# Optimization experiments

Measured on AMD Instinct MI355X. Metric: run time of the kernel, lower is better.

The kernel has to match this reference:

```python
import jax, jax.numpy as jnp
import numpy as np

B = 16384      # batch of samples
D = 65         # inps columns: 64 input spins + 1 output spin y
NA = 64        # auxiliary (threshold) spins
N = D + NA     # spins entering vspin expansion: 129
M = N + N * (N - 1) // 2  # degree-<=2 spin monomials: 8385
GAMMA = 1.0

# pairwise index pattern (i < j), computed once at trace time
_II, _JJ = np.triu_indices(N, k=1)


def batch_vspin(b):
    # b: [B, N] -> [B, N + N(N-1)/2]: linear terms then all pairwise products b_i*b_j (i<j)
    return jnp.concatenate([b, b[:, _II] * b[:, _JJ]], axis=-1)


def setup_inputs() -> dict:
    key = jax.random.key(0)
    k1, k2, k3, k4 = jax.random.split(key, 4)
    inps = jax.random.normal(k1, (B, D), dtype=jnp.float32)
    thresh_w = jax.random.normal(k2, (NA, D), dtype=jnp.float32) * 0.1
    thresh_b = jax.random.normal(k3, (NA,), dtype=jnp.float32) * 0.1
    main_w = jax.random.normal(k4, (1, M), dtype=jnp.float32) * 0.02
    return {"inps": inps, "thresh_w": thresh_w, "thresh_b": thresh_b, "main_w": main_w}


def reference(inps, thresh_w, thresh_b, main_w):
    inps = inps.astype(jnp.float32)
    x = inps[:, :-1]                      # [B, D-1]
    y = inps[:, -1:]                      # [B, 1]
    i_right = jnp.concatenate([x, y], axis=-1)    # [B, D]
    i_wrong = jnp.concatenate([x, -y], axis=-1)   # [B, D]

    w1 = i_right @ thresh_w.T + thresh_b          # [B, NA]
    w2 = i_wrong @ thresh_w.T + thresh_b          # [B, NA]
    t1 = jnp.tanh(GAMMA * w1)
    t2 = jnp.tanh(GAMMA * w2)

    b1 = jnp.concatenate([i_right, t1], axis=-1)  # [B, N]
    b2 = jnp.concatenate([i_wrong, t2], axis=-1)  # [B, N]
    v1 = batch_vspin(b1)                          # [B, M]
    v2 = batch_vspin(b2)                          # [B, M]

    diff = (v1 - v2) @ main_w.T + 1.0             # [B, 1]
    int_penalty = jnp.sum((GAMMA / 300.0) * ((1.0 - t1 ** 2) ** 2 + (1.0 - t2 ** 2) ** 2))
    neut_penalty = jnp.sum((t2 * w2 - t1 * w1) ** 2)
    return (diff, int_penalty, neut_penalty)
```

## Files before the change

### kernel.cpp

```cpp
#include <hip/hip_runtime.h>

#define B_SZ 16384
#define N_SP 129
#define GRID 1024
#define BLOCK 256

typedef _Float16 half8 __attribute__((ext_vector_type(8)));
typedef float float4v __attribute__((ext_vector_type(4)));

#define WS_TWY  6144
#define WS_QXY  6208
#define WS_QYT  6272
#define WS_LINT 6336
#define WS_LINY 6400
#define WS_P1   6464
#define WS_P2   7488

__device__ __forceinline__ int qidx(int i, int j) {
  return N_SP + i * (2 * N_SP - i - 1) / 2 + (j - i - 1);
}

__device__ __forceinline__ float fast_tanh(float x) {
  float xc = fminf(fmaxf(x, -15.f), 15.f);
  float e = __expf(2.f * xc);
  return 1.f - 2.f / (e + 1.f);
}

__global__ void setup_kernel(const float* __restrict__ mw, const float* __restrict__ tw,
                             float* __restrict__ wsf) {
  int t = blockIdx.x * blockDim.x + threadIdx.x;
  if (t < 12288) {
    int frag = t >> 9, e = t & 511;
    int lane = e >> 3, j = e & 7;
    int tbl = frag >> 3, tg = frag & 7;
    int kt = tg >> 2, g = tg & 3;
    int k = kt * 32 + (lane >> 4) * 8 + j;
    int n = (lane & 15) + 16 * g;
    float v;
    if (tbl == 0) {
      v = tw[n * 65 + k];
    } else if (tbl == 1) {
      v = mw[qidx(n, 65 + k)];
    } else {
      v = 0.f;
      if (n != k) {
        int a = n < k ? n : k, b = n < k ? k : n;
        v = mw[qidx(65 + a, 65 + b)];
      }
    }
    ((_Float16*)wsf)[t] = (_Float16)v;
  } else if (t < 12352) {
    int u = t - 12288; wsf[WS_TWY + u] = tw[u * 65 + 64];
  } else if (t < 12416) {
    int i = t - 12352; wsf[WS_QXY + i] = mw[qidx(i, 64)];
  } else if (t < 12480) {
    int u = t - 12416; wsf[WS_QYT + u] = mw[qidx(64, 65 + u)];
  } else if (t < 12544) {
    int u = t - 12480; wsf[WS_LINT + u] = mw[65 + u];
  } else if (t == 12544) {
    wsf[WS_LINY] = mw[64];
  }
}

__global__ __launch_bounds__(BLOCK, 4) void main_kernel(
    const float* __restrict__ inps, const float* __restrict__ tb,
    float* __restrict__ wsf, float* __restrict__ out) {
  __shared__ __align__(16) _Float16 s_frag[12288];
  __shared__ __align__(16) _Float16 s_x[1152];
  __shared__ __align__(16) _Float16 s_dt[1152];
  __shared__ float s_part[64];
  __shared__ float s_red[8];

  const int tid = threadIdx.x;
  const int l = tid & 63, wib = tid >> 6;
  const int b0 = blockIdx.x << 4;
  const int q = l >> 4, m = l & 15;
  const int u = (wib << 4) + m;

  {
    const float4* wsv = (const float4*)wsf;
    float4* dst = (float4*)s_frag;
#pragma unroll
    for (int i = 0; i < 6; i++) dst[tid + 256 * i] = wsv[tid + 256 * i];
  }
  const float twyv = wsf[WS_TWY + u];
  const float qxyv = wsf[WS_QXY + u];
  const float qytv = wsf[WS_QYT + u];
  const float lintv = wsf[WS_LINT + u];
  const float liny = wsf[WS_LINY];
  const float tbv = tb[u];

  {
    const float4* src4 = (const float4*)(inps + b0 * 65);
    float4 v = src4[tid];
#pragma unroll
    for (int c = 0; c < 4; c++) {
      unsigned idx = tid * 4 + c;
      unsigned row = idx / 65u, col = idx - row * 65u;
      s_x[row * 72 + col] = (_Float16)((const float*)&v)[c];
    }
    if (tid < 4) {
      float4 v2 = src4[256 + tid];
#pragma unroll
      for (int c = 0; c < 4; c++) {
        unsigned idx = (256 + tid) * 4 + c;
        unsigned row = idx / 65u, col = idx - row * 65u;
        s_x[row * 72 + col] = (_Float16)((const float*)&v2)[c];
      }
    }
  }
  __syncthreads();

  const half8* fragv = (const half8*)s_frag;

  half8 ax0 = *(const half8*)(s_x + m * 72 + q * 8);
  half8 ax1 = *(const half8*)(s_x + m * 72 + 32 + q * 8);

  float4v acc = {0.f, 0.f, 0.f, 0.f};
  acc = __builtin_amdgcn_mfma_f32_16x16x32_f16(ax0, fragv[(0 + wib) * 64 + l], acc, 0, 0, 0);
  acc = __builtin_amdgcn_mfma_f32_16x16x32_f16(ax1, fragv[(4 + wib) * 64 + l], acc, 0, 0, 0);

  float yv[4], dtv[4], stv[4];
  float pint = 0.f, pneut = 0.f;
#pragma unroll
  for (int r = 0; r < 4; r++) {
    yv[r] = (float)s_x[(q * 4 + r) * 72 + 64];
    float wpre = acc[r] + tbv;
    float w1 = wpre + twyv * yv[r];
    float w2 = wpre - twyv * yv[r];
    float t1 = fast_tanh(w1), t2 = fast_tanh(w2);
    dtv[r] = t1 - t2; stv[r] = t1 + t2;
    float a1 = 1.f - t1 * t1, a2 = 1.f - t2 * t2;
    pint += a1 * a1 + a2 * a2;
    float nv = t2 * w2 - t1 * w1;
    pneut += nv * nv;
    s_dt[(q * 4 + r) * 72 + u] = (_Float16)dtv[r];
  }
  __syncthreads();

  half8 ad0 = *(const half8*)(s_dt + m * 72 + q * 8);
  half8 ad1 = *(const half8*)(s_dt + m * 72 + 32 + q * 8);

  float4v rxt = {0.f, 0.f, 0.f, 0.f}, rtt = {0.f, 0.f, 0.f, 0.f};
  rxt = __builtin_amdgcn_mfma_f32_16x16x32_f16(ad0, fragv[(8 + wib) * 64 + l], rxt, 0, 0, 0);
  rxt = __builtin_amdgcn_mfma_f32_16x16x32_f16(ad1, fragv[(12 + wib) * 64 + l], rxt, 0, 0, 0);
  rtt = __builtin_amdgcn_mfma_f32_16x16x32_f16(ad0, fragv[(16 + wib) * 64 + l], rtt, 0, 0, 0);
  rtt = __builtin_amdgcn_mfma_f32_16x16x32_f16(ad1, fragv[(20 + wib) * 64 + l], rtt, 0, 0, 0);

  float creg[4];
#pragma unroll
  for (int r = 0; r < 4; r++) {
    float xv = (float)s_x[(q * 4 + r) * 72 + u];
    float c = xv * (2.f * yv[r] * qxyv + rxt[r])
            + yv[r] * stv[r] * qytv
            + 0.5f * stv[r] * rtt[r]
            + lintv * dtv[r];
    c += __shfl_xor(c, 1); c += __shfl_xor(c, 2);
    c += __shfl_xor(c, 4); c += __shfl_xor(c, 8);
    creg[r] = c;
  }
  if (m == 0) {
#pragma unroll
    for (int r = 0; r < 4; r++) s_part[wib * 16 + q * 4 + r] = creg[r];
  }

#pragma unroll
  for (int off = 1; off < 64; off <<= 1) {
    pint += __shfl_xor(pint, off);
    pneut += __shfl_xor(pneut, off);
  }
  if (l == 0) { s_red[wib] = pint; s_red[4 + wib] = pneut; }
  __syncthreads();

  if (tid < 16) {
    float c = s_part[tid] + s_part[16 + tid] + s_part[32 + tid] + s_part[48 + tid];
    float y = (float)s_x[tid * 72 + 64];
    out[b0 + tid] = 1.f + 2.f * y * liny + c;
  }
  if (tid == 0) {
    wsf[WS_P1 + blockIdx.x] = s_red[0] + s_red[1] + s_red[2] + s_red[3];
    wsf[WS_P2 + blockIdx.x] = s_red[4] + s_red[5] + s_red[6] + s_red[7];
  }
}

__global__ __launch_bounds__(1024) void reduce_kernel(const float* __restrict__ wsf,
                                                      float* __restrict__ out) {
  __shared__ float s[32];
  const int tid = threadIdx.x;
  float a = wsf[WS_P1 + tid];
  float b = wsf[WS_P2 + tid];
#pragma unroll
  for (int off = 1; off < 64; off <<= 1) {
    a += __shfl_xor(a, off);
    b += __shfl_xor(b, off);
  }
  const int w = tid >> 6, l = tid & 63;
  if (l == 0) { s[w] = a; s[16 + w] = b; }
  __syncthreads();
  if (tid == 0) {
    float sa = 0.f, sb = 0.f;
#pragma unroll
    for (int i = 0; i < 16; i++) { sa += s[i]; sb += s[16 + i]; }
    out[B_SZ] = sa * (1.f / 300.f);
    out[B_SZ + 1] = sb;
  }
}

extern "C" void kernel_launch(void* const* d_in, const int* in_sizes, int n_in,
                              void* d_out, int out_size, void* d_ws, size_t ws_size,
                              hipStream_t stream) {
  const float* inps = (const float*)d_in[0];
  const float* tw   = (const float*)d_in[1];
  const float* tb   = (const float*)d_in[2];
  const float* mw   = (const float*)d_in[3];
  float* out = (float*)d_out;
  float* wsf = (float*)d_ws;
  setup_kernel<<<50, 256, 0, stream>>>(mw, tw, wsf);
  main_kernel<<<GRID, BLOCK, 0, stream>>>(inps, tb, wsf, out);
  reduce_kernel<<<1, 1024, 0, stream>>>(wsf, out);
}
```

Baseline: 68.85 us.

## Fuse final reduction into main kernel via atomic ticket and async LDS loads

Removes the separate single-block reduce kernel. The last main-kernel block to finish, found through an atomic ticket counter, sums the per-block penalty partials itself. The fragment table now sits in device globals and is copied straight into LDS with global_load_lds, so it no longer passes through registers. This saves one kernel launch and its tail latency, at the cost of atomics and a global counter that must be reset correctly for every later call.

After: 87.24 us. +26.7%, slower.

```diff
diff --git a/kernel.cpp b/kernel.cpp
--- a/kernel.cpp
+++ b/kernel.cpp
@@ -8,13 +8,15 @@
 typedef _Float16 half8 __attribute__((ext_vector_type(8)));
 typedef float float4v __attribute__((ext_vector_type(4)));
 
-#define WS_TWY  6144
-#define WS_QXY  6208
-#define WS_QYT  6272
-#define WS_LINT 6336
-#define WS_LINY 6400
-#define WS_P1   6464
-#define WS_P2   7488
+__device__ __align__(16) _Float16 g_frag[12288];
+__device__ float g_twy[64];
+__device__ float g_qxy[64];
+__device__ float g_qyt[64];
+__device__ float g_lint[64];
+__device__ float g_liny_v;
+__device__ float g_p1[GRID];
+__device__ float g_p2[GRID];
+__device__ unsigned g_ticket = 0;
 
 __device__ __forceinline__ int qidx(int i, int j) {
   return N_SP + i * (2 * N_SP - i - 1) / 2 + (j - i - 1);
@@ -26,8 +28,7 @@
   return 1.f - 2.f / (e + 1.f);
 }
 
-__global__ void setup_kernel(const float* __restrict__ mw, const float* __restrict__ tw,
-                             float* __restrict__ wsf) {
+__global__ void setup_kernel(const float* __restrict__ mw, const float* __restrict__ tw) {
   int t = blockIdx.x * blockDim.x + threadIdx.x;
   if (t < 12288) {
     int frag = t >> 9, e = t & 511;
@@ -48,28 +49,29 @@
         v = mw[qidx(65 + a, 65 + b)];
       }
     }
-    ((_Float16*)wsf)[t] = (_Float16)v;
+    g_frag[t] = (_Float16)v;
   } else if (t < 12352) {
-    int u = t - 12288; wsf[WS_TWY + u] = tw[u * 65 + 64];
+    int u = t - 12288; g_twy[u] = tw[u * 65 + 64];
   } else if (t < 12416) {
-    int i = t - 12352; wsf[WS_QXY + i] = mw[qidx(i, 64)];
+    int i = t - 12352; g_qxy[i] = mw[qidx(i, 64)];
   } else if (t < 12480) {
-    int u = t - 12416; wsf[WS_QYT + u] = mw[qidx(64, 65 + u)];
+    int u = t - 12416; g_qyt[u] = mw[qidx(64, 65 + u)];
   } else if (t < 12544) {
-    int u = t - 12480; wsf[WS_LINT + u] = mw[65 + u];
+    int u = t - 12480; g_lint[u] = mw[65 + u];
   } else if (t == 12544) {
-    wsf[WS_LINY] = mw[64];
+    g_liny_v = mw[64];
   }
 }
 
 __global__ __launch_bounds__(BLOCK, 4) void main_kernel(
     const float* __restrict__ inps, const float* __restrict__ tb,
-    float* __restrict__ wsf, float* __restrict__ out) {
+    float* __restrict__ out) {
   __shared__ __align__(16) _Float16 s_frag[12288];
   __shared__ __align__(16) _Float16 s_x[1152];
   __shared__ __align__(16) _Float16 s_dt[1152];
   __shared__ float s_part[64];
   __shared__ float s_red[8];
+  __shared__ bool s_last;
 
   const int tid = threadIdx.x;
   const int l = tid & 63, wib = tid >> 6;
@@ -78,16 +80,20 @@
   const int u = (wib << 4) + m;
 
   {
-    const float4* wsv = (const float4*)wsf;
-    float4* dst = (float4*)s_frag;
-#pragma unroll
-    for (int i = 0; i < 6; i++) dst[tid + 256 * i] = wsv[tid + 256 * i];
-  }
-  const float twyv = wsf[WS_TWY + u];
-  const float qxyv = wsf[WS_QXY + u];
-  const float qytv = wsf[WS_QYT + u];
-  const float lintv = wsf[WS_LINT + u];
-  const float liny = wsf[WS_LINY];
+    const char* src = (const char*)g_frag;
+#pragma unroll
+    for (int i = 0; i < 6; i++) {
+      __builtin_amdgcn_global_load_lds(
+          (const __attribute__((address_space(1))) void*)(src + (tid + 256 * i) * 16),
+          (__attribute__((address_space(3))) void*)(s_frag + (wib * 64 + 256 * i) * 8),
+          16, 0, 0);
+    }
+  }
+  const float twyv = g_twy[u];
+  const float qxyv = g_qxy[u];
+  const float qytv = g_qyt[u];
+  const float lintv = g_lint[u];
+  const float liny = g_liny_v;
   const float tbv = tb[u];
 
   {
@@ -178,31 +184,35 @@
     out[b0 + tid] = 1.f + 2.f * y * liny + c;
   }
   if (tid == 0) {
-    wsf[WS_P1 + blockIdx.x] = s_red[0] + s_red[1] + s_red[2] + s_red[3];
-    wsf[WS_P2 + blockIdx.x] = s_red[4] + s_red[5] + s_red[6] + s_red[7];
-  }
-}
-
-__global__ __launch_bounds__(1024) void reduce_kernel(const float* __restrict__ wsf,
-                                                      float* __restrict__ out) {
-  __shared__ float s[32];
-  const int tid = threadIdx.x;
-  float a = wsf[WS_P1 + tid];
-  float b = wsf[WS_P2 + tid];
-#pragma unroll
-  for (int off = 1; off < 64; off <<= 1) {
-    a += __shfl_xor(a, off);
-    b += __shfl_xor(b, off);
-  }
-  const int w = tid >> 6, l = tid & 63;
-  if (l == 0) { s[w] = a; s[16 + w] = b; }
-  __syncthreads();
-  if (tid == 0) {
-    float sa = 0.f, sb = 0.f;
-#pragma unroll
-    for (int i = 0; i < 16; i++) { sa += s[i]; sb += s[16 + i]; }
-    out[B_SZ] = sa * (1.f / 300.f);
-    out[B_SZ + 1] = sb;
+    float bp1 = s_red[0] + s_red[1] + s_red[2] + s_red[3];
+    float bp2 = s_red[4] + s_red[5] + s_red[6] + s_red[7];
+    __hip_atomic_store(&g_p1[blockIdx.x], bp1, __ATOMIC_RELAXED, __HIP_MEMORY_SCOPE_AGENT);
+    __hip_atomic_store(&g_p2[blockIdx.x], bp2, __ATOMIC_RELAXED, __HIP_MEMORY_SCOPE_AGENT);
+    unsigned old = __hip_atomic_fetch_add(&g_ticket, 1u, __ATOMIC_ACQ_REL,
+                                          __HIP_MEMORY_SCOPE_AGENT);
+    s_last = (old == GRID - 1);
+  }
+  __syncthreads();
+
+  if (s_last) {
+    float a = 0.f, b = 0.f;
+#pragma unroll
+    for (int k = 0; k < 4; k++) {
+      a += __hip_atomic_load(&g_p1[tid + 256 * k], __ATOMIC_RELAXED, __HIP_MEMORY_SCOPE_AGENT);
+      b += __hip_atomic_load(&g_p2[tid + 256 * k], __ATOMIC_RELAXED, __HIP_MEMORY_SCOPE_AGENT);
+    }
+#pragma unroll
+    for (int off = 1; off < 64; off <<= 1) {
+      a += __shfl_xor(a, off);
+      b += __shfl_xor(b, off);
+    }
+    if (l == 0) { s_part[wib] = a; s_part[4 + wib] = b; }
+    __syncthreads();
+    if (tid == 0) {
+      out[B_SZ] = (s_part[0] + s_part[1] + s_part[2] + s_part[3]) * (1.f / 300.f);
+      out[B_SZ + 1] = s_part[4] + s_part[5] + s_part[6] + s_part[7];
+      __hip_atomic_store(&g_ticket, 0u, __ATOMIC_RELAXED, __HIP_MEMORY_SCOPE_AGENT);
+    }
   }
 }
 
@@ -214,8 +224,7 @@
   const float* tb   = (const float*)d_in[2];
   const float* mw   = (const float*)d_in[3];
   float* out = (float*)d_out;
-  float* wsf = (float*)d_ws;
-  setup_kernel<<<50, 256, 0, stream>>>(mw, tw, wsf);
-  main_kernel<<<GRID, BLOCK, 0, stream>>>(inps, tb, wsf, out);
-  reduce_kernel<<<1, 1024, 0, stream>>>(wsf, out);
-}
+  (void)d_ws; (void)ws_size;
+  setup_kernel<<<50, 256, 0, stream>>>(mw, tw);
+  main_kernel<<<GRID, BLOCK, 0, stream>>>(inps, tb, out);
+}
```

## Drop setup kernel; load MFMA B-fragments directly from global into registers

Applied to the files above, without the earlier changes.

Removes the separate setup kernel that pre-packed fp16 weight fragments into the workspace. Each thread now gathers and converts its own B-operand fragments straight from the raw weight arrays into registers, so the 24KB shared-memory staging copy goes away. This saves one launch and frees LDS, which may allow more blocks per CU. The cost is scattered, uncoalesced global gathers that every block repeats, though these should mostly hit in cache. Per-block partial sums move to __device__ globals.

After: 71.73 us. 4.2% more time.

```diff
diff --git a/kernel.cpp b/kernel.cpp
--- a/kernel.cpp
+++ b/kernel.cpp
@@ -8,13 +8,8 @@
 typedef _Float16 half8 __attribute__((ext_vector_type(8)));
 typedef float float4v __attribute__((ext_vector_type(4)));
 
-#define WS_TWY  6144
-#define WS_QXY  6208
-#define WS_QYT  6272
-#define WS_LINT 6336
-#define WS_LINY 6400
-#define WS_P1   6464
-#define WS_P2   7488
+__device__ float g_p1[GRID];
+__device__ float g_p2[GRID];
 
 __device__ __forceinline__ int qidx(int i, int j) {
   return N_SP + i * (2 * N_SP - i - 1) / 2 + (j - i - 1);
@@ -26,46 +21,10 @@
   return 1.f - 2.f / (e + 1.f);
 }
 
-__global__ void setup_kernel(const float* __restrict__ mw, const float* __restrict__ tw,
-                             float* __restrict__ wsf) {
-  int t = blockIdx.x * blockDim.x + threadIdx.x;
-  if (t < 12288) {
-    int frag = t >> 9, e = t & 511;
-    int lane = e >> 3, j = e & 7;
-    int tbl = frag >> 3, tg = frag & 7;
-    int kt = tg >> 2, g = tg & 3;
-    int k = kt * 32 + (lane >> 4) * 8 + j;
-    int n = (lane & 15) + 16 * g;
-    float v;
-    if (tbl == 0) {
-      v = tw[n * 65 + k];
-    } else if (tbl == 1) {
-      v = mw[qidx(n, 65 + k)];
-    } else {
-      v = 0.f;
-      if (n != k) {
-        int a = n < k ? n : k, b = n < k ? k : n;
-        v = mw[qidx(65 + a, 65 + b)];
-      }
-    }
-    ((_Float16*)wsf)[t] = (_Float16)v;
-  } else if (t < 12352) {
-    int u = t - 12288; wsf[WS_TWY + u] = tw[u * 65 + 64];
-  } else if (t < 12416) {
-    int i = t - 12352; wsf[WS_QXY + i] = mw[qidx(i, 64)];
-  } else if (t < 12480) {
-    int u = t - 12416; wsf[WS_QYT + u] = mw[qidx(64, 65 + u)];
-  } else if (t < 12544) {
-    int u = t - 12480; wsf[WS_LINT + u] = mw[65 + u];
-  } else if (t == 12544) {
-    wsf[WS_LINY] = mw[64];
-  }
-}
-
 __global__ __launch_bounds__(BLOCK, 4) void main_kernel(
-    const float* __restrict__ inps, const float* __restrict__ tb,
-    float* __restrict__ wsf, float* __restrict__ out) {
-  __shared__ __align__(16) _Float16 s_frag[12288];
+    const float* __restrict__ inps, const float* __restrict__ tw,
+    const float* __restrict__ tb, const float* __restrict__ mw,
+    float* __restrict__ out) {
   __shared__ __align__(16) _Float16 s_x[1152];
   __shared__ __align__(16) _Float16 s_dt[1152];
   __shared__ float s_part[64];
@@ -78,19 +37,6 @@
   const int u = (wib << 4) + m;
 
   {
-    const float4* wsv = (const float4*)wsf;
-    float4* dst = (float4*)s_frag;
-#pragma unroll
-    for (int i = 0; i < 6; i++) dst[tid + 256 * i] = wsv[tid + 256 * i];
-  }
-  const float twyv = wsf[WS_TWY + u];
-  const float qxyv = wsf[WS_QXY + u];
-  const float qytv = wsf[WS_QYT + u];
-  const float lintv = wsf[WS_LINT + u];
-  const float liny = wsf[WS_LINY];
-  const float tbv = tb[u];
-
-  {
     const float4* src4 = (const float4*)(inps + b0 * 65);
     float4 v = src4[tid];
 #pragma unroll
@@ -109,16 +55,54 @@
       }
     }
   }
-  __syncthreads();
-
-  const half8* fragv = (const half8*)s_frag;
+
+  half8 bf0, bf1, bf2, bf3, bf4, bf5;
+  {
+    const int k0 = q * 8;
+    const int k1 = 32 + q * 8;
+    const int tw_base = u * 65;
+    const int q1_base = qidx(u, 65);
+#pragma unroll
+    for (int j = 0; j < 8; j++) bf0[j] = (_Float16)tw[tw_base + k0 + j];
+#pragma unroll
+    for (int j = 0; j < 8; j++) bf1[j] = (_Float16)tw[tw_base + k1 + j];
+#pragma unroll
+    for (int j = 0; j < 8; j++) bf2[j] = (_Float16)mw[q1_base + k0 + j];
+#pragma unroll
+    for (int j = 0; j < 8; j++) bf3[j] = (_Float16)mw[q1_base + k1 + j];
+#pragma unroll
+    for (int j = 0; j < 8; j++) {
+      int k = k0 + j;
+      int a = u < k ? u : k, b = u < k ? k : u;
+      int idx = (u == k) ? 0 : qidx(65 + a, 65 + b);
+      float v = mw[idx];
+      bf4[j] = (_Float16)((u == k) ? 0.f : v);
+    }
+#pragma unroll
+    for (int j = 0; j < 8; j++) {
+      int k = k1 + j;
+      int a = u < k ? u : k, b = u < k ? k : u;
+      int idx = (u == k) ? 0 : qidx(65 + a, 65 + b);
+      float v = mw[idx];
+      bf5[j] = (_Float16)((u == k) ? 0.f : v);
+    }
+  }
+
+  const float twyv = tw[u * 65 + 64];
+  const float qxyv = mw[qidx(u, 64)];
+  const float qytv = mw[qidx(64, 65 + u)];
+  const float lintv = mw[65 + u];
+  const float liny = mw[64];
+  const float tbv = tb[u];
+
+  __syncthreads();
 
   half8 ax0 = *(const half8*)(s_x + m * 72 + q * 8);
   half8 ax1 = *(const half8*)(s_x + m * 72 + 32 + q * 8);
 
   float4v acc = {0.f, 0.f, 0.f, 0.f};
-  acc = __builtin_amdgcn_mfma_f32_16x16x32_f16(ax0, fragv[(0 + wib) * 64 + l], acc, 0, 0, 0);
-  acc = __builtin_amdgcn_mfma_f32_16x16x32_f16(ax1, fragv[(4 + wib) * 64 + l], acc, 0, 0, 0);
+  acc = __builtin_amdgcn_mfma_f32_16x16x32_f16(ax0, bf0, acc, 0, 0, 0);
+  acc = __builtin_amdgcn_mfma_f32_16x16x32_f16(ax1, bf1, acc, 0, 0, 0);
 
   float yv[4], dtv[4], stv[4];
   float pint = 0.f, pneut = 0.f;
@@ -142,10 +126,10 @@
   half8 ad1 = *(const half8*)(s_dt + m * 72 + 32 + q * 8);
 
   float4v rxt = {0.f, 0.f, 0.f, 0.f}, rtt = {0.f, 0.f, 0.f, 0.f};
-  rxt = __builtin_amdgcn_mfma_f32_16x16x32_f16(ad0, fragv[(8 + wib) * 64 + l], rxt, 0, 0, 0);
-  rxt = __builtin_amdgcn_mfma_f32_16x16x32_f16(ad1, fragv[(12 + wib) * 64 + l], rxt, 0, 0, 0);
-  rtt = __builtin_amdgcn_mfma_f32_16x16x32_f16(ad0, fragv[(16 + wib) * 64 + l], rtt, 0, 0, 0);
-  rtt = __builtin_amdgcn_mfma_f32_16x16x32_f16(ad1, fragv[(20 + wib) * 64 + l], rtt, 0, 0, 0);
+  rxt = __builtin_amdgcn_mfma_f32_16x16x32_f16(ad0, bf2, rxt, 0, 0, 0);
+  rxt = __builtin_amdgcn_mfma_f32_16x16x32_f16(ad1, bf3, rxt, 0, 0, 0);
+  rtt = __builtin_amdgcn_mfma_f32_16x16x32_f16(ad0, bf4, rtt, 0, 0, 0);
+  rtt = __builtin_amdgcn_mfma_f32_16x16x32_f16(ad1, bf5, rtt, 0, 0, 0);
 
   float creg[4];
 #pragma unroll
@@ -178,17 +162,16 @@
     out[b0 + tid] = 1.f + 2.f * y * liny + c;
   }
   if (tid == 0) {
-    wsf[WS_P1 + blockIdx.x] = s_red[0] + s_red[1] + s_red[2] + s_red[3];
-    wsf[WS_P2 + blockIdx.x] = s_red[4] + s_red[5] + s_red[6] + s_red[7];
-  }
-}
-
-__global__ __launch_bounds__(1024) void reduce_kernel(const float* __restrict__ wsf,
-                                                      float* __restrict__ out) {
+    g_p1[blockIdx.x] = s_red[0] + s_red[1] + s_red[2] + s_red[3];
+    g_p2[blockIdx.x] = s_red[4] + s_red[5] + s_red[6] + s_red[7];
+  }
+}
+
+__global__ __launch_bounds__(1024) void reduce_kernel(float* __restrict__ out) {
   __shared__ float s[32];
   const int tid = threadIdx.x;
-  float a = wsf[WS_P1 + tid];
-  float b = wsf[WS_P2 + tid];
+  float a = g_p1[tid];
+  float b = g_p2[tid];
 #pragma unroll
   for (int off = 1; off < 64; off <<= 1) {
     a += __shfl_xor(a, off);
@@ -214,8 +197,7 @@
   const float* tb   = (const float*)d_in[2];
   const float* mw   = (const float*)d_in[3];
   float* out = (float*)d_out;
-  float* wsf = (float*)d_ws;
-  setup_kernel<<<50, 256, 0, stream>>>(mw, tw, wsf);
-  main_kernel<<<GRID, BLOCK, 0, stream>>>(inps, tb, wsf, out);
-  reduce_kernel<<<1, 1024, 0, stream>>>(wsf, out);
-}
+  (void)d_ws; (void)ws_size;
+  main_kernel<<<GRID, BLOCK, 0, stream>>>(inps, tw, tb, mw, out);
+  reduce_kernel<<<1, 1024, 0, stream>>>(out);
+}
```
